# Kernel tuning notes

Measured on AMD Instinct MI355X. Metric: run time of the kernel, lower is better.

The kernel has to match this reference:

```python
import jax, jax.numpy as jnp
import numpy as np

NHEADS = 16

def setup_inputs() -> dict:
    key = jax.random.key(0)
    ks = jax.random.split(key, 5)
    C = 1024
    d = C // NHEADS
    x  = jax.random.normal(ks[0], (2, 2048, C), dtype=jnp.float32)
    sc = 1.0 / np.sqrt(C)
    wq = jax.random.normal(ks[1], (C, C), dtype=jnp.float32) * sc
    wk = jax.random.normal(ks[2], (C, C), dtype=jnp.float32) * sc
    wv = jax.random.normal(ks[3], (C, C), dtype=jnp.float32) * sc
    wo = jax.random.normal(ks[4], (d, C), dtype=jnp.float32) * (1.0 / np.sqrt(d))
    return {"x": x, "wq": wq, "wk": wk, "wv": wv, "wo": wo}

def reference(x, wq, wk, wv, wo):
    B, T, C = x.shape
    H = NHEADS
    d = C // H

    def split_heads(y):
        return y.reshape(B, T, H, d).transpose(0, 2, 1, 3)  # [B,H,T,d]

    Q = split_heads(x @ wq)
    K = split_heads(x @ wk)
    V = split_heads(x @ wv)

    # scores[b,h,q,k]
    prod = jnp.einsum('bhqd,bhkd->bhqk', Q, K) / np.sqrt(d)

    # ALiBi bias: offset[h, q, k] = (k - q) * 2**(-8*(h+1)/H)
    idx = jnp.arange(T)
    slopes = jnp.exp2(-8.0 * (jnp.arange(H, dtype=jnp.float32) + 1.0) / H)
    bias = (idx[None, :] - idx[:, None]).astype(x.dtype) * slopes[:, None, None]
    prod = prod + bias[None]

    # causal tril mask: keep k <= q
    keep = idx[None, :] <= idx[:, None]  # [T_q, T_k]
    prod = jnp.where(keep[None, None], prod, -jnp.inf)

    # NOTE: original uses F.softmax(prod, 2) -> softmax over the QUERY axis.
    attention_weights = jax.nn.softmax(prod, axis=2)
    attention_output = jnp.einsum('bhqk,bhkd->bhqd', attention_weights, V)

    # per-head wo projection then sum over heads == (sum over heads) @ wo (linear)
    outputs = attention_output.sum(axis=1) @ wo  # [B,T,C]
    return x + outputs
```

## Files before the change

kernel.cpp:

```cpp
#include <hip/hip_runtime.h>
#include <math.h>

#define NB 2
#define NH 16
#define NT 2048
#define ND 64
#define NC 1024
#define L2E 1.44269504f

typedef __attribute__((ext_vector_type(4))) float f32x4;
typedef __attribute__((ext_vector_type(8))) short short8;
typedef __attribute__((ext_vector_type(4))) short short4_t;
typedef __attribute__((ext_vector_type(8))) unsigned short ushort8;
typedef __attribute__((ext_vector_type(4))) unsigned short ushort4_t;

__device__ const int WTAB[16] = {2,2,3,3,4,5,6,8,11,15,21,29,32,32,32,32};

#define GLOAD_LDS(gp, lp)                                                \
    __builtin_amdgcn_global_load_lds(                                    \
        (const __attribute__((address_space(1))) void*)(gp),             \
        (__attribute__((address_space(3))) void*)(lp), 16, 0, 0)

__device__ __forceinline__ int sigma_p(int p) {
    return 4 * ((p >> 3) & 3) + (p & 3) + 16 * ((p >> 2) & 1) + 32 * (p >> 5);
}

__device__ __forceinline__ unsigned short f2bf(float f) {
    unsigned u = __builtin_bit_cast(unsigned, f);
    unsigned r = (u + 0x7FFFu + ((u >> 16) & 1u)) >> 16;
    return (unsigned short)r;
}

__device__ __forceinline__ float bf2f(unsigned short s) {
    return __builtin_bit_cast(float, (unsigned)s << 16);
}

__device__ __forceinline__ unsigned cvtpk_bf16(float lo, float hi) {
    unsigned r;
    asm("v_cvt_pk_bf16_f32 %0, %1, %2" : "=v"(r) : "v"(lo), "v"(hi));
    return r;
}

__device__ __forceinline__ f32x4 mfma16(short8 a, short8 b, f32x4 c) {
    return __builtin_amdgcn_mfma_f32_16x16x32_bf16(a, b, c, 0, 0, 0);
}

__device__ __forceinline__ short8 frag_load(const unsigned short* rowp, int g, int half) {
    short8 v;
    short4_t lo = *(const short4_t*)(rowp + 4 * g + 32 * half);
    short4_t hi = *(const short4_t*)(rowp + 4 * g + 16 + 32 * half);
    #pragma unroll
    for (int j = 0; j < 4; ++j) { v[j] = lo[j]; v[4 + j] = hi[j]; }
    return v;
}

__device__ __forceinline__ short8 frag_g(const unsigned short* rowp, int g, int half) {
    return *(const short8*)(rowp + 8 * g + 32 * half);
}

__device__ __forceinline__ short8 frag_swz128(const unsigned short* tile, int row, int g, int half) {
    const char* p = (const char*)tile + row * 128 + (((g + 4 * half) ^ (row & 7)) << 4);
    return *(const short8*)p;
}

__global__ __launch_bounds__(256) void cvt_x(const float* __restrict__ src,
                                             unsigned short* __restrict__ dst, int n4) {
    int i = blockIdx.x * 256 + threadIdx.x;
    if (i >= n4) return;
    const int blk = i >> 4, c4 = i & 15;
    const int gg = (c4 >> 1) & 3, bb = c4 & 1, hh = c4 >> 3;
    f32x4 v = ((const f32x4*)src)[blk * 16 + gg + 4 * bb + 8 * hh];
    ushort4_t o;
    #pragma unroll
    for (int j = 0; j < 4; ++j) o[j] = f2bf(v[j]);
    ((ushort4_t*)dst)[i] = o;
}

__global__ __launch_bounds__(256) void cvtW(const float* __restrict__ w0,
                                            const float* __restrict__ w1,
                                            const float* __restrict__ w2,
                                            const float* __restrict__ w3,
                                            unsigned short* __restrict__ Wt_all,
                                            unsigned short* __restrict__ Wot) {
    __shared__ __align__(16) float T[64][68];
    const int z = blockIdx.z;
    const int tid = threadIdx.x;
    if (z == 3) {
        if (blockIdx.x != 0) return;
        const int n0 = blockIdx.y * 64;
        #pragma unroll
        for (int p = 0; p < 4; ++p) {
            int r = 16 * p + (tid >> 4);
            int c = (tid & 15) * 4;
            *(f32x4*)&T[r][c] = *(const f32x4*)&w3[(size_t)r * NC + n0 + c];
        }
        __syncthreads();
        const int nr = tid >> 2, kc = (tid & 3) * 16;
        ushort8 o0, o1;
        #pragma unroll
        for (int j = 0; j < 8; ++j) { o0[j] = f2bf(T[kc + j][nr]); o1[j] = f2bf(T[kc + 8 + j][nr]); }
        unsigned short* q = Wot + (size_t)(n0 + nr) * ND + kc;
        *(ushort8*)q       = o0;
        *(ushort8*)(q + 8) = o1;
        return;
    }
    const float* W = (z == 0) ? w0 : ((z == 1) ? w1 : w2);
    unsigned short* Wt = Wt_all + (size_t)z * NC * NC;
    const int k0 = blockIdx.x * 64, n0 = blockIdx.y * 64;
    #pragma unroll
    for (int p = 0; p < 4; ++p) {
        int r = 16 * p + (tid >> 4);
        int c = (tid & 15) * 4;
        *(f32x4*)&T[r][c] = *(const f32x4*)&W[(size_t)(k0 + r) * NC + n0 + c];
    }
    __syncthreads();
    const int nr = tid >> 2, kc = (tid & 3) * 16;
    ushort8 o0, o1;
    #pragma unroll
    for (int j = 0; j < 8; ++j) o0[j] = f2bf(T[sigma_p(kc + j)][nr]);
    #pragma unroll
    for (int j = 0; j < 8; ++j) o1[j] = f2bf(T[sigma_p(kc + 8 + j)][nr]);
    unsigned short* q = Wt + (size_t)(n0 + nr) * NC + k0 + kc;
    *(ushort8*)q       = o0;
    *(ushort8*)(q + 8) = o1;
}

__global__ __launch_bounds__(256) void gemm_qkv(const unsigned short* __restrict__ Xh,
                                                const unsigned short* __restrict__ Wt_all,
                                                unsigned short* __restrict__ qk_dst,
                                                unsigned short* __restrict__ Vt) {
    __shared__ __align__(16) unsigned short Xs[2][8192];
    __shared__ __align__(16) unsigned short Ws[2][8192];
    const int tid = threadIdx.x;
    const int lane = tid & 63, w = tid >> 6;
    const int g = lane >> 4, l15 = lane & 15;
    const int wr = w >> 1, wc = w & 1;
    const int subrow = lane >> 3;
    const int src_off = (((lane & 7) ^ subrow) << 4);
    const int m0 = blockIdx.x * 128;
    const int which = blockIdx.y >> 3;
    const int n0 = (blockIdx.y & 7) * 128;
    const unsigned short* Wt = Wt_all + (size_t)which * NC * NC;

    f32x4 acc[4][4] = {};

    auto stage = [&](int buf, int kk) {
        #pragma unroll
        for (int i = 0; i < 4; ++i) {
            const int r0 = 8 * w + 32 * i;
            const char* xs = (const char*)Xh + (((size_t)(m0 + r0 + subrow) * NC + kk) << 1) + src_off;
            GLOAD_LDS(xs, (char*)&Xs[buf][r0 * 64]);
            const char* ws = (const char*)Wt + (((size_t)(n0 + r0 + subrow) * NC + kk) << 1) + src_off;
            GLOAD_LDS(ws, (char*)&Ws[buf][r0 * 64]);
        }
    };

    stage(0, 0);
    asm volatile("s_waitcnt vmcnt(0)" ::: "memory");
    __builtin_amdgcn_s_barrier();
    int cur = 0;

    for (int kk = 0; kk < NC; kk += 64) {
        if (kk + 64 < NC) stage(cur ^ 1, kk + 64);
        short8 a[4][2], b[4][2];
        #pragma unroll
        for (int mr = 0; mr < 4; ++mr) {
            a[mr][0] = frag_swz128(Xs[cur], 64 * wr + 16 * mr + l15, g, 0);
            a[mr][1] = frag_swz128(Xs[cur], 64 * wr + 16 * mr + l15, g, 1);
        }
        #pragma unroll
        for (int nc = 0; nc < 4; ++nc) {
            b[nc][0] = frag_swz128(Ws[cur], 64 * wc + 16 * nc + l15, g, 0);
            b[nc][1] = frag_swz128(Ws[cur], 64 * wc + 16 * nc + l15, g, 1);
        }
        #pragma unroll
        for (int mr = 0; mr < 4; ++mr)
            #pragma unroll
            for (int nc = 0; nc < 4; ++nc) {
                acc[mr][nc] = mfma16(a[mr][0], b[nc][0], acc[mr][nc]);
                acc[mr][nc] = mfma16(a[mr][1], b[nc][1], acc[mr][nc]);
            }
        asm volatile("s_waitcnt vmcnt(0)" ::: "memory");
        __builtin_amdgcn_s_barrier();
        cur ^= 1;
    }

    if (which < 2) {
        unsigned short* dst = qk_dst + (size_t)which * (NB * NH * NT * ND);
        #pragma unroll
        for (int mr = 0; mr < 4; ++mr) {
            #pragma unroll
            for (int nc = 0; nc < 4; ++nc) {
                const int n = n0 + 64 * wc + 16 * nc + l15;
                const int hh = n >> 6;
                const int dd = 32 * (nc >> 1) + 8 * (l15 >> 2) + 4 * (nc & 1) + (l15 & 3);
                #pragma unroll
                for (int r = 0; r < 4; ++r) {
                    const int m = m0 + 64 * wr + 16 * mr + 4 * g + r;
                    const int bb = m >> 11, tt = m & (NT - 1);
                    dst[(((size_t)bb * NH + hh) * NT + tt) * ND + dd] = f2bf(acc[mr][nc][r]);
                }
            }
        }
    } else {
        #pragma unroll
        for (int mr = 0; mr < 4; ++mr) {
            const int m = m0 + 64 * wr + 16 * mr + 4 * g;
            const int bb = m >> 11, tt = m & (NT - 1);
            const int tbase = (tt & ~63) + 32 * (mr >> 1) + 8 * g + 4 * (mr & 1);
            #pragma unroll
            for (int nc = 0; nc < 4; ++nc) {
                const int n = n0 + 64 * wc + 16 * nc + l15;
                const int hh = n >> 6, dd = n & 63;
                ushort4_t o;
                #pragma unroll
                for (int r = 0; r < 4; ++r) o[r] = f2bf(acc[mr][nc][r]);
                *(ushort4_t*)&Vt[(((size_t)bb * NH + hh) * ND + dd) * NT + tbase] = o;
            }
        }
    }
}

__global__ __launch_bounds__(256, 4) void colstats(const unsigned short* __restrict__ Qh,
                                                   const unsigned short* __restrict__ Kh,
                                                   float* __restrict__ Lc) {
    __shared__ __align__(16) unsigned short Qs[3][4096];
    const int tid = threadIdx.x;
    const int lane = tid & 63, w = tid >> 6;
    const int g = lane >> 4, l15 = lane & 15;
    const int subrow = lane >> 3;
    const int src_off = (((lane & 7) ^ subrow) << 4);
    const int lin = blockIdx.x + 32 * blockIdx.y;
    const int xcd = lin & 7, idx = lin >> 3;
    const int slot = idx & 3;
    const int j = idx >> 2;
    const int hh = (slot & 1) ? (15 - xcd) : xcd;
    const int bh = ((slot >> 1) << 4) + hh;
    const float slL2 = exp2f(-0.5f * (float)(hh + 1)) * L2E;
    const float C1 = 0.125f * L2E;
    const float s16 = 16.f * slL2;
    const int Wt = WTAB[hh];
    const int qtend = min(32, j + Wt);

    const unsigned short* kr = Kh + ((size_t)bh * NT + 64 * j + 16 * w + l15) * ND;
    const short8 ak0 = frag_g(kr, g, 0), ak1 = frag_g(kr, g, 1);
    const int k0 = 64 * j + 16 * w + 4 * g;

    const char* Qbase = (const char*)(Qh + (size_t)bh * NT * ND);
    auto stage = [&](int buf, int qt) {
        const char* qs = Qbase + (size_t)(64 * qt + 16 * w + subrow) * 128 + src_off;
        char* qd = (char*)&Qs[buf][16 * w * 64];
        GLOAD_LDS(qs, qd);
        GLOAD_LDS(qs + 1024, qd + 1024);
    };

    f32x4 acc = {};
    float rs[4];
    #pragma unroll
    for (int r = 0; r < 4; ++r) rs[r] = (float)r * slL2;

    stage(0, j);
    if (j + 1 < qtend) stage(1, j + 1);
    int cur = 0, nxt = 2;

    for (int qt = j; qt < qtend; ++qt) {
        if (qt + 1 < qtend) asm volatile("s_waitcnt vmcnt(2)" ::: "memory");
        else                asm volatile("s_waitcnt vmcnt(0)" ::: "memory");
        __builtin_amdgcn_s_barrier();
        if (qt + 2 < qtend) stage(nxt, qt + 2);
        const unsigned short* tile = Qs[cur];
        short8 qf[8];
        #pragma unroll
        for (int q4 = 0; q4 < 4; ++q4) {
            qf[2 * q4]     = frag_swz128(tile, 16 * q4 + l15, g, 0);
            qf[2 * q4 + 1] = frag_swz128(tile, 16 * q4 + l15, g, 1);
        }
        float b0 = (float)(k0 - 64 * qt - l15) * slL2;
        const bool mask = (qt == j);
        #pragma unroll
        for (int q4 = 0; q4 < 4; ++q4) {
            f32x4 d = {};
            __builtin_amdgcn_s_setprio(1);
            d = mfma16(ak0, qf[2 * q4], d);
            d = mfma16(ak1, qf[2 * q4 + 1], d);
            __builtin_amdgcn_s_setprio(0);
            #pragma unroll
            for (int r = 0; r < 4; ++r) {
                float e = exp2f(fmaf(d[r], C1, b0 + rs[r]));
                if (mask && (16 * q4 + l15 < 16 * w + 4 * g + r)) e = 0.f;
                acc[r] += e;
            }
            b0 -= s16;
        }
        cur = (cur == 2) ? 0 : cur + 1;
        nxt = (nxt == 2) ? 0 : nxt + 1;
    }
    #pragma unroll
    for (int off = 1; off <= 8; off <<= 1)
        #pragma unroll
        for (int r = 0; r < 4; ++r) acc[r] += __shfl_xor(acc[r], off);
    if (l15 == 0) {
        #pragma unroll
        for (int r = 0; r < 4; ++r)
            Lc[(size_t)bh * NT + k0 + r] = acc[r];
    }
}

__global__ __launch_bounds__(256) void scale_v(const float* __restrict__ Lc,
                                               unsigned short* __restrict__ Vt) {
    const int i = blockIdx.x * 256 + threadIdx.x;
    const int bh = i >> 15;
    const int tpos4 = (i & 511) * 4;
    const int tlog = (tpos4 & ~63) + sigma_p(tpos4 & 63);
    f32x4 a = *(const f32x4*)(Lc + (size_t)bh * NT + tlog);
    ushort4_t v = ((const ushort4_t*)Vt)[i];
    ushort4_t o;
    #pragma unroll
    for (int j = 0; j < 4; ++j)
        o[j] = f2bf(bf2f(v[j]) / a[j]);
    ((ushort4_t*)Vt)[i] = o;
}

__global__ __launch_bounds__(256, 3) void attn_pv(const unsigned short* __restrict__ Qh,
                                                  const unsigned short* __restrict__ Kh,
                                                  const unsigned short* __restrict__ Vt,
                                                  float* __restrict__ att) {
    __shared__ __align__(16) unsigned short Ks[3][4096];
    __shared__ __align__(16) unsigned short Vs[3][4096];
    const int tid = threadIdx.x;
    const int lane = tid & 63, w = tid >> 6;
    const int g = lane >> 4, l15 = lane & 15;
    const int subrow = lane >> 3;
    const int src_off = (((lane & 7) ^ subrow) << 4);
    const int lin = blockIdx.x + 32 * blockIdx.y;
    const int xcd = lin & 7, idx = lin >> 3;
    const int slot = idx & 3;
    const int j = 31 - (idx >> 2);
    const int hh = (slot & 1) ? (15 - xcd) : xcd;
    const int bh = ((slot >> 1) << 4) + hh;
    const int bb = bh >> 4;
    const float slL2 = exp2f(-0.5f * (float)(hh + 1)) * L2E;
    const float C1 = 0.125f * L2E;
    const float s16 = 16.f * slL2;
    const int Wt = WTAB[hh];
    const int ktmin = max(0, j - Wt + 1);

    const int q = 64 * j + 16 * w + l15;
    short8 bq0, bq1;
    {
        const unsigned short* qr = Qh + ((size_t)bh * NT + q) * ND;
        bq0 = frag_g(qr, g, 0);
        bq1 = frag_g(qr, g, 1);
    }
    float rs[4];
    #pragma unroll
    for (int r = 0; r < 4; ++r) rs[r] = (float)r * slL2;

    auto stageKV = [&](int buf, int K0) {
        const char* ksrc = (const char*)Kh + (size_t)((size_t)bh * NT + K0 + 16 * w + subrow) * 128 + src_off;
        char* kdst = (char*)&Ks[buf][16 * w * 64];
        GLOAD_LDS(ksrc, kdst);
        GLOAD_LDS(ksrc + 1024, kdst + 1024);
        const char* vsrc = (const char*)Vt + ((((size_t)bh * ND + 16 * w + subrow) * NT + K0) << 1) + src_off;
        char* vdst = (char*)&Vs[buf][16 * w * 64];
        GLOAD_LDS(vsrc, vdst);
        GLOAD_LDS(vsrc + 8 * NT * 2, vdst + 1024);
    };

    stageKV(0, 64 * ktmin);
    if (ktmin < j) stageKV(1, 64 * (ktmin + 1));
    int cur = 0, nxt = 2;

    f32x4 o[4] = {};

    for (int kt = ktmin; kt <= j; ++kt) {
        if (kt < j) asm volatile("s_waitcnt vmcnt(4)" ::: "memory");
        else        asm volatile("s_waitcnt vmcnt(0)" ::: "memory");
        __builtin_amdgcn_s_barrier();
        if (kt + 2 <= j) stageKV(nxt, 64 * (kt + 2));
        const int K0 = 64 * kt;
        short8 kf[8], vf[8];
        #pragma unroll
        for (int s4 = 0; s4 < 4; ++s4) {
            kf[2 * s4]     = frag_swz128(Ks[cur], 16 * s4 + l15, g, 0);
            kf[2 * s4 + 1] = frag_swz128(Ks[cur], 16 * s4 + l15, g, 1);
            vf[2 * s4]     = frag_swz128(Vs[cur], 16 * s4 + l15, g, 0);
            vf[2 * s4 + 1] = frag_swz128(Vs[cur], 16 * s4 + l15, g, 1);
        }
        f32x4 pacc[4];
        __builtin_amdgcn_s_setprio(1);
        #pragma unroll
        for (int s4 = 0; s4 < 4; ++s4) {
            f32x4 d = {};
            d = mfma16(kf[2 * s4], bq0, d);
            d = mfma16(kf[2 * s4 + 1], bq1, d);
            pacc[s4] = d;
        }
        __builtin_amdgcn_s_setprio(0);
        union { unsigned u[4]; short8 s; } pa[2];
        float b = (float)(K0 + 4 * g - q) * slL2;
        const bool mask = (kt == j);
        #pragma unroll
        for (int s4 = 0; s4 < 4; ++s4) {
            float p[4];
            #pragma unroll
            for (int r = 0; r < 4; ++r)
                p[r] = exp2f(fmaf(pacc[s4][r], C1, b + rs[r]));
            if (mask) {
                #pragma unroll
                for (int r = 0; r < 4; ++r)
                    if (K0 + 16 * s4 + 4 * g + r > q) p[r] = 0.f;
            }
            pa[s4 >> 1].u[2 * (s4 & 1)]     = cvtpk_bf16(p[0], p[1]);
            pa[s4 >> 1].u[2 * (s4 & 1) + 1] = cvtpk_bf16(p[2], p[3]);
            b += s16;
        }
        __builtin_amdgcn_s_setprio(1);
        #pragma unroll
        for (int n = 0; n < 4; ++n) {
            o[n] = mfma16(pa[0].s, vf[2 * n], o[n]);
            o[n] = mfma16(pa[1].s, vf[2 * n + 1], o[n]);
        }
        __builtin_amdgcn_s_setprio(0);
        cur = (cur == 2) ? 0 : cur + 1;
        nxt = (nxt == 2) ? 0 : nxt + 1;
    }
    #pragma unroll
    for (int n = 0; n < 4; ++n) {
        #pragma unroll
        for (int r = 0; r < 4; ++r) {
            att[(((size_t)bb * NT + 64 * j + 16 * w + 4 * g + r) * NH + hh) * ND + 16 * n + l15] = o[n][r];
        }
    }
}

__global__ __launch_bounds__(256) void headsum(const float* __restrict__ att,
                                               unsigned short* __restrict__ A) {
    const int row = blockIdx.x * 16 + (threadIdx.x >> 4);
    const int d0 = (threadIdx.x & 15) * 4;
    const float* p = att + (size_t)row * (NH * ND) + d0;
    f32x4 s = {};
    #pragma unroll
    for (int h = 0; h < NH; ++h)
        s += *(const f32x4*)(p + h * ND);
    ushort4_t o;
    #pragma unroll
    for (int j = 0; j < 4; ++j) o[j] = f2bf(s[j]);
    *(ushort4_t*)&A[(size_t)row * ND + d0] = o;
}

__global__ __launch_bounds__(256) void out_proj(const float* __restrict__ x,
                                                const unsigned short* __restrict__ A,
                                                const unsigned short* __restrict__ Wot,
                                                float* __restrict__ out) {
    const int tid = threadIdx.x;
    const int lane = tid & 63, w = tid >> 6;
    const int g = lane >> 4, l15 = lane & 15;
    const int m0 = blockIdx.x * 64, n0 = blockIdx.y * 64;

    const unsigned short* ar = A + (size_t)(m0 + 16 * w + l15) * ND;
    short8 a0 = frag_load(ar, g, 0);
    short8 a1 = frag_load(ar, g, 1);

    f32x4 acc[4] = {};
    #pragma unroll
    for (int ns = 0; ns < 4; ++ns) {
        const unsigned short* br = Wot + (size_t)(n0 + 16 * ns + l15) * ND;
        acc[ns] = mfma16(a0, frag_load(br, g, 0), acc[ns]);
        acc[ns] = mfma16(a1, frag_load(br, g, 1), acc[ns]);
    }
    #pragma unroll
    for (int ns = 0; ns < 4; ++ns) {
        #pragma unroll
        for (int r = 0; r < 4; ++r) {
            int m = m0 + 16 * w + 4 * g + r;
            int n = n0 + 16 * ns + l15;
            out[(size_t)m * NC + n] = x[(size_t)m * NC + n] + acc[ns][r];
        }
    }
}

extern "C" void kernel_launch(void* const* d_in, const int* in_sizes, int n_in,
                              void* d_out, int out_size, void* d_ws, size_t ws_size,
                              hipStream_t stream) {
    const float* x  = (const float*)d_in[0];
    const float* wq = (const float*)d_in[1];
    const float* wk = (const float*)d_in[2];
    const float* wv = (const float*)d_in[3];
    const float* wo = (const float*)d_in[4];
    float* out = (float*)d_out;

    const size_t MB = 1u << 20;
    const size_t KB = 1u << 10;
    unsigned char* w8 = (unsigned char*)d_ws;
    unsigned short* Xh  = (unsigned short*)(w8);
    unsigned short* Wta = (unsigned short*)(w8 + 8 * MB);
    unsigned short* Qh  = (unsigned short*)(w8 + 16 * MB);
    unsigned short* Kh  = (unsigned short*)(w8 + 24 * MB);
    unsigned short* Vt  = (unsigned short*)(w8 + 32 * MB);
    float*          att = (float*)(w8 + 40 * MB);
    float*          Lc  = (float*)(w8 + 56 * MB);
    unsigned short* A   = (unsigned short*)(w8 + 56 * MB + 512 * KB);
    unsigned short* Wot = (unsigned short*)(w8 + 57 * MB);

    cvt_x<<<(NB * NT * NC) / 1024, 256, 0, stream>>>(x, Xh, (NB * NT * NC) / 4);
    cvtW<<<dim3(16, 16, 4), 256, 0, stream>>>(wq, wk, wv, wo, Wta, Wot);

    gemm_qkv<<<dim3(32, 24), 256, 0, stream>>>(Xh, Wta, Qh, Vt);

    colstats<<<dim3(32, 32), 256, 0, stream>>>(Qh, Kh, Lc);
    scale_v<<<(32 * ND * NT / 4) / 256, 256, 0, stream>>>(Lc, Vt);
    attn_pv<<<dim3(32, 32), 256, 0, stream>>>(Qh, Kh, Vt, att);

    headsum<<<(NB * NT) / 16, 256, 0, stream>>>(att, A);
    out_proj<<<dim3(64, 16), 256, 0, stream>>>(x, A, Wot, out);
}
```

Before: 141.5 us.

## Triple-buffer QKV GEMM, fuse V scaling into colstats, store attention in bf16

The QKV GEMM moves from a 2-stage, 64-wide-K pipeline to a 3-stage pipeline with 32-wide K tiles, a new swizzle, a partial vmcnt wait and raised MFMA priority. This aims to overlap loads with compute and raise occupancy. The separate scale_v kernel is removed: colstats now divides its V tile by the column sums held in shared memory, saving a launch and a round trip through Lc. The per-head attention output is stored as bf16 instead of fp32, halving headsum's traffic at some precision cost.

```diff
diff --git a/kernel.cpp b/kernel.cpp
--- a/kernel.cpp
+++ b/kernel.cpp
@@ -60,6 +60,11 @@
 
 __device__ __forceinline__ short8 frag_swz128(const unsigned short* tile, int row, int g, int half) {
     const char* p = (const char*)tile + row * 128 + (((g + 4 * half) ^ (row & 7)) << 4);
+    return *(const short8*)p;
+}
+
+__device__ __forceinline__ short8 frag_swz32(const unsigned short* tile, int row, int g) {
+    const char* p = (const char*)tile + row * 64 + (((g ^ ((row >> 1) & 3))) << 4);
     return *(const short8*)p;
 }
 
@@ -125,64 +130,63 @@
     *(ushort8*)(q + 8) = o1;
 }
 
-__global__ __launch_bounds__(256) void gemm_qkv(const unsigned short* __restrict__ Xh,
-                                                const unsigned short* __restrict__ Wt_all,
-                                                unsigned short* __restrict__ qk_dst,
-                                                unsigned short* __restrict__ Vt) {
-    __shared__ __align__(16) unsigned short Xs[2][8192];
-    __shared__ __align__(16) unsigned short Ws[2][8192];
+__global__ __launch_bounds__(256, 3) void gemm_qkv(const unsigned short* __restrict__ Xh,
+                                                   const unsigned short* __restrict__ Wt_all,
+                                                   unsigned short* __restrict__ qk_dst,
+                                                   unsigned short* __restrict__ Vt) {
+    __shared__ __align__(16) unsigned short Xs[3][4096];
+    __shared__ __align__(16) unsigned short Ws[3][4096];
     const int tid = threadIdx.x;
     const int lane = tid & 63, w = tid >> 6;
     const int g = lane >> 4, l15 = lane & 15;
     const int wr = w >> 1, wc = w & 1;
-    const int subrow = lane >> 3;
-    const int src_off = (((lane & 7) ^ subrow) << 4);
     const int m0 = blockIdx.x * 128;
     const int which = blockIdx.y >> 3;
     const int n0 = (blockIdx.y & 7) * 128;
     const unsigned short* Wt = Wt_all + (size_t)which * NC * NC;
 
+    const int sr[2] = { (0 * 256 + w * 64 + lane) >> 2, (1 * 256 + w * 64 + lane) >> 2 };
+    const int sc[2] = { ((0 * 256 + w * 64 + lane) & 3) ^ ((sr[0] >> 1) & 3),
+                        ((1 * 256 + w * 64 + lane) & 3) ^ ((sr[1] >> 1) & 3) };
+
     f32x4 acc[4][4] = {};
 
-    auto stage = [&](int buf, int kk) {
-        #pragma unroll
-        for (int i = 0; i < 4; ++i) {
-            const int r0 = 8 * w + 32 * i;
-            const char* xs = (const char*)Xh + (((size_t)(m0 + r0 + subrow) * NC + kk) << 1) + src_off;
-            GLOAD_LDS(xs, (char*)&Xs[buf][r0 * 64]);
-            const char* ws = (const char*)Wt + (((size_t)(n0 + r0 + subrow) * NC + kk) << 1) + src_off;
-            GLOAD_LDS(ws, (char*)&Ws[buf][r0 * 64]);
+    auto stage = [&](int buf, int kt) {
+        const size_t kb = (size_t)kt * 64;
+        #pragma unroll
+        for (int i = 0; i < 2; ++i) {
+            const char* xs = (const char*)Xh + (size_t)(m0 + sr[i]) * 2048 + kb + (sc[i] << 4);
+            GLOAD_LDS(xs, (char*)&Xs[buf][(i * 256 + w * 64) * 8]);
+            const char* ws = (const char*)Wt + (size_t)(n0 + sr[i]) * 2048 + kb + (sc[i] << 4);
+            GLOAD_LDS(ws, (char*)&Ws[buf][(i * 256 + w * 64) * 8]);
         }
     };
 
     stage(0, 0);
-    asm volatile("s_waitcnt vmcnt(0)" ::: "memory");
-    __builtin_amdgcn_s_barrier();
-    int cur = 0;
-
-    for (int kk = 0; kk < NC; kk += 64) {
-        if (kk + 64 < NC) stage(cur ^ 1, kk + 64);
-        short8 a[4][2], b[4][2];
-        #pragma unroll
-        for (int mr = 0; mr < 4; ++mr) {
-            a[mr][0] = frag_swz128(Xs[cur], 64 * wr + 16 * mr + l15, g, 0);
-            a[mr][1] = frag_swz128(Xs[cur], 64 * wr + 16 * mr + l15, g, 1);
-        }
-        #pragma unroll
-        for (int nc = 0; nc < 4; ++nc) {
-            b[nc][0] = frag_swz128(Ws[cur], 64 * wc + 16 * nc + l15, g, 0);
-            b[nc][1] = frag_swz128(Ws[cur], 64 * wc + 16 * nc + l15, g, 1);
-        }
+    stage(1, 1);
+    int cur = 0, nxt = 2;
+
+    for (int kt = 0; kt < 32; ++kt) {
+        if (kt < 31) asm volatile("s_waitcnt vmcnt(4)" ::: "memory");
+        else         asm volatile("s_waitcnt vmcnt(0)" ::: "memory");
+        __builtin_amdgcn_s_barrier();
+        if (kt + 2 < 32) stage(nxt, kt + 2);
+        short8 a[4], b[4];
+        #pragma unroll
+        for (int mr = 0; mr < 4; ++mr)
+            a[mr] = frag_swz32(Xs[cur], 64 * wr + 16 * mr + l15, g);
+        #pragma unroll
+        for (int nc = 0; nc < 4; ++nc)
+            b[nc] = frag_swz32(Ws[cur], 64 * wc + 16 * nc + l15, g);
+        __builtin_amdgcn_s_setprio(1);
         #pragma unroll
         for (int mr = 0; mr < 4; ++mr)
             #pragma unroll
-            for (int nc = 0; nc < 4; ++nc) {
-                acc[mr][nc] = mfma16(a[mr][0], b[nc][0], acc[mr][nc]);
-                acc[mr][nc] = mfma16(a[mr][1], b[nc][1], acc[mr][nc]);
-            }
-        asm volatile("s_waitcnt vmcnt(0)" ::: "memory");
-        __builtin_amdgcn_s_barrier();
-        cur ^= 1;
+            for (int nc = 0; nc < 4; ++nc)
+                acc[mr][nc] = mfma16(a[mr], b[nc], acc[mr][nc]);
+        __builtin_amdgcn_s_setprio(0);
+        cur = (cur == 2) ? 0 : cur + 1;
+        nxt = (nxt == 2) ? 0 : nxt + 1;
     }
 
     if (which < 2) {
@@ -223,8 +227,9 @@
 
 __global__ __launch_bounds__(256, 4) void colstats(const unsigned short* __restrict__ Qh,
                                                    const unsigned short* __restrict__ Kh,
-                                                   float* __restrict__ Lc) {
+                                                   unsigned short* __restrict__ Vt) {
     __shared__ __align__(16) unsigned short Qs[3][4096];
+    __shared__ __align__(16) float Ssum[64];
     const int tid = threadIdx.x;
     const int lane = tid & 63, w = tid >> 6;
     const int g = lane >> 4, l15 = lane & 15;
@@ -301,30 +306,30 @@
         for (int r = 0; r < 4; ++r) acc[r] += __shfl_xor(acc[r], off);
     if (l15 == 0) {
         #pragma unroll
-        for (int r = 0; r < 4; ++r)
-            Lc[(size_t)bh * NT + k0 + r] = acc[r];
-    }
-}
-
-__global__ __launch_bounds__(256) void scale_v(const float* __restrict__ Lc,
-                                               unsigned short* __restrict__ Vt) {
-    const int i = blockIdx.x * 256 + threadIdx.x;
-    const int bh = i >> 15;
-    const int tpos4 = (i & 511) * 4;
-    const int tlog = (tpos4 & ~63) + sigma_p(tpos4 & 63);
-    f32x4 a = *(const f32x4*)(Lc + (size_t)bh * NT + tlog);
-    ushort4_t v = ((const ushort4_t*)Vt)[i];
-    ushort4_t o;
-    #pragma unroll
-    for (int j = 0; j < 4; ++j)
-        o[j] = f2bf(bf2f(v[j]) / a[j]);
-    ((ushort4_t*)Vt)[i] = o;
+        for (int r = 0; r < 4; ++r) Ssum[16 * w + 4 * g + r] = acc[r];
+    }
+    __syncthreads();
+
+    unsigned short* Vst = Vt + (size_t)bh * ND * NT + 64 * j;
+    #pragma unroll
+    for (int it = 0; it < 4; ++it) {
+        const int c = 256 * it + tid;
+        const int d = c >> 4;
+        const int tp4 = (c & 15) * 4;
+        f32x4 s = *(const f32x4*)&Ssum[sigma_p(tp4)];
+        unsigned short* p = Vst + (size_t)d * NT + tp4;
+        ushort4_t v = *(const ushort4_t*)p;
+        ushort4_t o;
+        #pragma unroll
+        for (int r = 0; r < 4; ++r) o[r] = f2bf(bf2f(v[r]) / s[r]);
+        *(ushort4_t*)p = o;
+    }
 }
 
 __global__ __launch_bounds__(256, 3) void attn_pv(const unsigned short* __restrict__ Qh,
                                                   const unsigned short* __restrict__ Kh,
                                                   const unsigned short* __restrict__ Vt,
-                                                  float* __restrict__ att) {
+                                                  unsigned short* __restrict__ att) {
     __shared__ __align__(16) unsigned short Ks[3][4096];
     __shared__ __align__(16) unsigned short Vs[3][4096];
     const int tid = threadIdx.x;
@@ -429,23 +434,26 @@
     for (int n = 0; n < 4; ++n) {
         #pragma unroll
         for (int r = 0; r < 4; ++r) {
-            att[(((size_t)bb * NT + 64 * j + 16 * w + 4 * g + r) * NH + hh) * ND + 16 * n + l15] = o[n][r];
-        }
-    }
-}
-
-__global__ __launch_bounds__(256) void headsum(const float* __restrict__ att,
+            att[(((size_t)bb * NT + 64 * j + 16 * w + 4 * g + r) * NH + hh) * ND + 16 * n + l15] = f2bf(o[n][r]);
+        }
+    }
+}
+
+__global__ __launch_bounds__(256) void headsum(const unsigned short* __restrict__ att,
                                                unsigned short* __restrict__ A) {
     const int row = blockIdx.x * 16 + (threadIdx.x >> 4);
     const int d0 = (threadIdx.x & 15) * 4;
-    const float* p = att + (size_t)row * (NH * ND) + d0;
+    const unsigned short* p = att + (size_t)row * (NH * ND) + d0;
     f32x4 s = {};
     #pragma unroll
-    for (int h = 0; h < NH; ++h)
-        s += *(const f32x4*)(p + h * ND);
+    for (int h = 0; h < NH; ++h) {
+        ushort4_t v = *(const ushort4_t*)(p + h * ND);
+        #pragma unroll
+        for (int jj = 0; jj < 4; ++jj) s[jj] += bf2f(v[jj]);
+    }
     ushort4_t o;
     #pragma unroll
-    for (int j = 0; j < 4; ++j) o[j] = f2bf(s[j]);
+    for (int jj = 0; jj < 4; ++jj) o[jj] = f2bf(s[jj]);
     *(ushort4_t*)&A[(size_t)row * ND + d0] = o;
 }
 
@@ -498,18 +506,16 @@
     unsigned short* Qh  = (unsigned short*)(w8 + 16 * MB);
     unsigned short* Kh  = (unsigned short*)(w8 + 24 * MB);
     unsigned short* Vt  = (unsigned short*)(w8 + 32 * MB);
-    float*          att = (float*)(w8 + 40 * MB);
-    float*          Lc  = (float*)(w8 + 56 * MB);
-    unsigned short* A   = (unsigned short*)(w8 + 56 * MB + 512 * KB);
-    unsigned short* Wot = (unsigned short*)(w8 + 57 * MB);
+    unsigned short* att = (unsigned short*)(w8 + 40 * MB);
+    unsigned short* A   = (unsigned short*)(w8 + 48 * MB);
+    unsigned short* Wot = (unsigned short*)(w8 + 48 * MB + 512 * KB);
 
     cvt_x<<<(NB * NT * NC) / 1024, 256, 0, stream>>>(x, Xh, (NB * NT * NC) / 4);
     cvtW<<<dim3(16, 16, 4), 256, 0, stream>>>(wq, wk, wv, wo, Wta, Wot);
 
     gemm_qkv<<<dim3(32, 24), 256, 0, stream>>>(Xh, Wta, Qh, Vt);
 
-    colstats<<<dim3(32, 32), 256, 0, stream>>>(Qh, Kh, Lc);
-    scale_v<<<(32 * ND * NT / 4) / 256, 256, 0, stream>>>(Lc, Vt);
+    colstats<<<dim3(32, 32), 256, 0, stream>>>(Qh, Kh, Vt);
     attn_pv<<<dim3(32, 32), 256, 0, stream>>>(Qh, Kh, Vt, att);
 
     headsum<<<(NB * NT) / 16, 256, 0, stream>>>(att, A);
```

Result: faster. 127.1 us, median of 2 (-10.2%).
